# Optimization experiments

Measured on AMD Instinct MI355X. Metric: run time of the kernel, lower is better.

Reference implementation:

```python
import jax, jax.numpy as jnp
import numpy as np
from jax import lax

B, T, N, H = 2048, 128, 128, 256  # batch, timesteps, input_size (drivers), hidden_size


def setup_inputs() -> dict:
    key = jax.random.key(0)
    k = jax.random.split(key, 7)
    s = 0.05
    return {
        "input_data": jax.random.normal(k[0], (B, T, N), jnp.float32),
        "w_ih": jax.random.normal(k[1], (4 * H, N), jnp.float32) * s,   # PyTorch weight_ih_l0
        "w_hh": jax.random.normal(k[2], (4 * H, H), jnp.float32) * s,   # PyTorch weight_hh_l0
        "b_ih": jax.random.normal(k[3], (4 * H,), jnp.float32) * s,
        "b_hh": jax.random.normal(k[4], (4 * H,), jnp.float32) * s,
        "w_attn": jax.random.normal(k[5], (2 * H + T,), jnp.float32) * s,  # attn_linear weight (out=1)
        "b_attn": jax.random.normal(k[6], (1,), jnp.float32) * s,
    }


def reference(input_data, w_ih, w_hh, b_ih, b_hh, w_attn, b_attn):
    b, t_steps, n = input_data.shape
    h_dim = w_hh.shape[1]
    # Split attention weight: [h | c | driver-series] parts of the concat feature.
    w_h = w_attn[:h_dim]
    w_c = w_attn[h_dim:2 * h_dim]
    w_x = w_attn[2 * h_dim:]
    # Driver-series contribution to attn logits is time-invariant: [B, N]
    precomp = jnp.einsum("btn,t->bn", input_data, w_x)
    bias = b_attn[0]
    gate_bias = b_ih + b_hh

    xs = jnp.transpose(input_data, (1, 0, 2))  # [T, B, N]

    def step(carry, x_t):
        h, c = carry  # [B, H] each
        # hidden/cell are broadcast identically across the N drivers -> scalar per batch
        s = h @ w_h + c @ w_c                       # [B]
        logits = s[:, None] + precomp + bias        # [B, N]
        attn = jax.nn.softmax(logits, axis=1)       # [B, N]
        wx = attn * x_t                             # weighted input, [B, N]
        # PyTorch LSTM cell: gates ordered i, f, g, o
        gates = wx @ w_ih.T + h @ w_hh.T + gate_bias  # [B, 4H]
        i, f, g, o = jnp.split(gates, 4, axis=1)
        c_new = jax.nn.sigmoid(f) * c + jax.nn.sigmoid(i) * jnp.tanh(g)
        h_new = jax.nn.sigmoid(o) * jnp.tanh(c_new)
        return (h_new, c_new), (wx, h_new)

    h0 = jnp.zeros((b, h_dim), input_data.dtype)
    c0 = jnp.zeros((b, h_dim), input_data.dtype)
    _, (ws, hs) = lax.scan(step, (h0, c0), xs)
    input_weighted = jnp.transpose(ws, (1, 0, 2))  # [B, T, N]
    input_encoded = jnp.transpose(hs, (1, 0, 2))   # [B, T, H]
    return input_weighted, input_encoded
```

## Files before the change

### kernel.cpp

```cpp
#include <hip/hip_runtime.h>
#include <hip/hip_bf16.h>


#define B_ 2048
#define T_ 128
#define N_ 128
#define H_ 256
#define RG_ 64

typedef float f32x4 __attribute__((ext_vector_type(4)));
typedef short bf16x8 __attribute__((ext_vector_type(8)));
typedef unsigned short u16;
typedef unsigned int u32;
typedef u32 u32x4 __attribute__((ext_vector_type(4)));

__device__ __forceinline__ u16 f2bf(float f) {
  unsigned int u = __float_as_uint(f);
  u += 0x7fffu + ((u >> 16) & 1u);
  return (u16)(u >> 16);
}
__device__ __forceinline__ float sigm(float x) { return 1.f / (1.f + __expf(-x)); }
__device__ __forceinline__ float tanh_(float x) {
  float e = __expf(2.f * x);
  return 1.f - 2.f / (e + 1.f);
}

__device__ __forceinline__ bf16x8 ld16_dev(const u16* p) {
  bf16x8 v;
  asm volatile("global_load_dwordx4 %0, %1, off sc0 sc1" : "=v"(v) : "v"(p));
  return v;
}
__device__ __forceinline__ void st16_dev(u16* p, bf16x8 v) {
  asm volatile("global_store_dwordx4 %0, %1, off sc0 sc1" :: "v"(p), "v"(v) : "memory");
}
__device__ __forceinline__ void st1_dev(unsigned char* p, u32 v) {
  asm volatile("global_store_byte %0, %1, off sc0 sc1" :: "v"(p), "v"(v) : "memory");
}
__device__ __forceinline__ u32x4 ld_flags(const unsigned char* p) {
  u32x4 f;
  asm volatile("global_load_dwordx4 %0, %1, off sc0 sc1\n\ts_waitcnt vmcnt(0)"
               : "=v"(f) : "v"(p) : "memory");
  return f;
}

__global__ __launch_bounds__(128) void attn_wx_kernel(
    const float* __restrict__ x, const float* __restrict__ w_attn,
    float* __restrict__ out0) {
  const int b = blockIdx.x;
  const int n = threadIdx.x;
  const float* xb = x + (size_t)b * (T_ * N_);
  __shared__ float red[N_];
  float xv[T_];
  float p = 0.f;
#pragma unroll
  for (int t = 0; t < T_; ++t) {
    xv[t] = xb[t * N_ + n];
    p += xv[t] * w_attn[2 * H_ + t];
  }
  red[n] = p;
  __syncthreads();
  float m = red[0];
  for (int i = 1; i < N_; ++i) m = fmaxf(m, red[i]);
  float e = __expf(p - m);
  __syncthreads();
  red[n] = e;
  __syncthreads();
  float s = 0.f;
  for (int i = 0; i < N_; ++i) s += red[i];
  const float a = e / s;
  float* ob = out0 + (size_t)b * (T_ * N_);
#pragma unroll
  for (int t = 0; t < T_; ++t) ob[t * N_ + n] = a * xv[t];
}

__global__ __launch_bounds__(256) void prepack_kernel(
    const float* __restrict__ w_ih, const float* __restrict__ w_hh,
    u16* __restrict__ wpk) {
  const int idx = blockIdx.x * 256 + threadIdx.x;
  const int j = idx & 7;
  const int l = (idx >> 3) & 63;
  const int rest = idx >> 9;
  const int kc = rest % 12;
  const int wq = rest / 12;
  const int q = wq & 3;
  const int g16 = wq >> 2;
  const int grow = q * H_ + g16 * 16 + (l & 15);
  const int k = kc * 32 + ((l >> 4) << 3) + j;
  const float v = (k < N_) ? w_ih[(size_t)grow * N_ + k]
                           : w_hh[(size_t)grow * H_ + (k - N_)];
  wpk[idx] = f2bf(v);
}

__global__ __launch_bounds__(256, 1) void lstm_kernel(
    const float* __restrict__ wx,
    const u16* __restrict__ wpk,
    const float* __restrict__ b_ih, const float* __restrict__ b_hh,
    float* __restrict__ out1,
    u16* __restrict__ hx,
    unsigned char* __restrict__ flags) {
  __shared__ u16 hsh[2][32][72];
  const int bid = blockIdx.x;
  const int rg = bid >> 2, cg = bid & 3;
  const int rb = rg * 32;
  const int tid  = threadIdx.x;
  const int w    = tid >> 6;
  const int lane = tid & 63;
  const int l15  = lane & 15;
  const int koff = (lane >> 4) << 3;
  const int g16  = cg * 4 + w;
  const int hcol = cg * 64 + w * 16 + l15;

  bf16x8 wfrag[4][12];
  {
    const u16* wp = wpk + (size_t)(g16 * 48) * 512 + (size_t)lane * 8;
#pragma unroll
    for (int q = 0; q < 4; ++q)
#pragma unroll
      for (int kc = 0; kc < 12; ++kc)
        wfrag[q][kc] = *(const bf16x8*)(wp + (size_t)(q * 12 + kc) * 512);
  }
  float bias[4];
#pragma unroll
  for (int q = 0; q < 4; ++q)
    bias[q] = b_ih[q * H_ + hcol] + b_hh[q * H_ + hcol];
  float creg[2][4] = {};

  unsigned char* flrow  = flags + rg * 16;
  unsigned char* myflag = flrow + cg * 4 + w;
  const int mtf = w >> 1, kclf = w & 1;

  f32x4 pf[2][4][2];
#pragma unroll
  for (int mt = 0; mt < 2; ++mt)
#pragma unroll
    for (int kc = 0; kc < 4; ++kc) {
      const float* p = wx + (size_t)(rb + mt * 16 + l15) * (T_ * N_)
                          + kc * 32 + koff;
      pf[mt][kc][0] = *(const f32x4*)p;
      pf[mt][kc][1] = *(const f32x4*)(p + 4);
    }

  for (int t = 0; t < T_; ++t) {
    f32x4 acc[2][4];
#pragma unroll
    for (int mt = 0; mt < 2; ++mt)
#pragma unroll
      for (int q = 0; q < 4; ++q)
        acc[mt][q] = (f32x4){bias[q], bias[q], bias[q], bias[q]};

#pragma unroll
    for (int kc = 0; kc < 4; ++kc)
#pragma unroll
      for (int mt = 0; mt < 2; ++mt) {
        f32x4 x0 = pf[mt][kc][0], x1 = pf[mt][kc][1];
        bf16x8 a;
        a[0] = (short)f2bf(x0[0]); a[1] = (short)f2bf(x0[1]);
        a[2] = (short)f2bf(x0[2]); a[3] = (short)f2bf(x0[3]);
        a[4] = (short)f2bf(x1[0]); a[5] = (short)f2bf(x1[1]);
        a[6] = (short)f2bf(x1[2]); a[7] = (short)f2bf(x1[3]);
#pragma unroll
        for (int q = 0; q < 4; ++q)
          acc[mt][q] = __builtin_amdgcn_mfma_f32_16x16x32_bf16(a, wfrag[q][kc], acc[mt][q], 0, 0, 0);
      }
    if (t + 1 < T_) {
#pragma unroll
      for (int mt = 0; mt < 2; ++mt)
#pragma unroll
        for (int kc = 0; kc < 4; ++kc) {
          const float* p = wx + (size_t)(rb + mt * 16 + l15) * (T_ * N_)
                              + (size_t)(t + 1) * N_ + kc * 32 + koff;
          pf[mt][kc][0] = *(const f32x4*)p;
          pf[mt][kc][1] = *(const f32x4*)(p + 4);
        }
    }

    if (t > 0) {
      while (true) {
        u32x4 f = ld_flags(flrow);
        int ok = 1;
#pragma unroll
        for (int i = 0; i < 4; ++i) {
          u32 v = f[i];
          ok &= ((v & 255u) >= (u32)t) & (((v >> 8) & 255u) >= (u32)t) &
                (((v >> 16) & 255u) >= (u32)t) & (((v >> 24) & 255u) >= (u32)t);
        }
        if (ok) break;
      }
      __builtin_amdgcn_sched_barrier(0);

      const u16* hxr = hx + ((size_t)(t & 1) * RG_ + rg) * (4 * 4 * 512);
      bf16x8 ah[2][8];
#pragma unroll
      for (int mt = 0; mt < 2; ++mt)
#pragma unroll
        for (int kc2 = 0; kc2 < 8; ++kc2) {
          const int pc = kc2 >> 1, kcl = kc2 & 1;
          if (pc == cg)
            ah[mt][kc2] = *(const bf16x8*)&hsh[t & 1][mt * 16 + l15][kcl * 32 + koff];
          else
            ah[mt][kc2] = ld16_dev(hxr + ((size_t)pc * 4 + (mt * 2 + kcl)) * 512
                                       + (size_t)lane * 8);
        }
      asm volatile("s_waitcnt vmcnt(0)" ::: "memory");
      __builtin_amdgcn_sched_barrier(0);
#pragma unroll
      for (int kc2 = 0; kc2 < 8; ++kc2)
#pragma unroll
        for (int q = 0; q < 4; ++q)
#pragma unroll
          for (int mt = 0; mt < 2; ++mt)
            acc[mt][q] = __builtin_amdgcn_mfma_f32_16x16x32_bf16(ah[mt][kc2], wfrag[q][4 + kc2], acc[mt][q], 0, 0, 0);
    }

    const int nxt = (t + 1) & 1;
#pragma unroll
    for (int mt = 0; mt < 2; ++mt)
#pragma unroll
      for (int rr = 0; rr < 4; ++rr) {
        const float gi = acc[mt][0][rr];
        const float gf = acc[mt][1][rr];
        const float gg = acc[mt][2][rr];
        const float go = acc[mt][3][rr];
        const float c = sigm(gf) * creg[mt][rr] + sigm(gi) * tanh_(gg);
        creg[mt][rr] = c;
        const float h = sigm(go) * tanh_(c);
        const int row = mt * 16 + ((lane >> 4) << 2) + rr;
        out1[(size_t)(rb + row) * (T_ * H_) + (size_t)t * H_ + hcol] = h;
        hsh[nxt][row][w * 16 + l15] = f2bf(h);
      }
    __syncthreads();

    {
      bf16x8 fv = *(const bf16x8*)&hsh[nxt][mtf * 16 + l15][kclf * 32 + koff];
      u16* dst = hx + (((size_t)nxt * RG_ + rg) * 4 + cg) * (4 * 512)
                    + (size_t)w * 512 + (size_t)lane * 8;
      st16_dev(dst, fv);
      asm volatile("s_waitcnt vmcnt(0)" ::: "memory");
      if (lane == 0) st1_dev(myflag, (u32)(t + 1));
    }
  }
}

extern "C" void kernel_launch(void* const* d_in, const int* in_sizes, int n_in,
                              void* d_out, int out_size, void* d_ws, size_t ws_size,
                              hipStream_t stream) {
  const float* x      = (const float*)d_in[0];
  const float* w_ih   = (const float*)d_in[1];
  const float* w_hh   = (const float*)d_in[2];
  const float* b_ih   = (const float*)d_in[3];
  const float* b_hh   = (const float*)d_in[4];
  const float* w_attn = (const float*)d_in[5];

  float* out0 = (float*)d_out;
  float* out1 = out0 + (size_t)B_ * T_ * N_;

  unsigned char* flags = (unsigned char*)d_ws;
  u16* wpk = (u16*)((char*)d_ws + 16384);
  u16* hx  = (u16*)((char*)d_ws + 16384 + 786432);

  hipMemsetAsync(d_ws, 0, RG_ * 16, stream);
  prepack_kernel<<<dim3(1536), dim3(256), 0, stream>>>(w_ih, w_hh, wpk);
  attn_wx_kernel<<<dim3(B_), dim3(N_), 0, stream>>>(x, w_attn, out0);
  lstm_kernel<<<dim3(256), dim3(256), 0, stream>>>(out0, wpk, b_ih, b_hh,
                                                   out1, hx, flags);
}
```

Measured before the change: 961.2 us.

## Halve rows per LSTM block, double grid, stage inputs and peer h via LDS

Each LSTM block now handles 16 batch rows instead of 32, so the grid grows from 256 to 512 blocks at two blocks per CU. The next step's wx input is staged through a swizzled double-buffered LDS tile. Peer h fragments are loaded once per block by three waves into shared memory, not by every wave. The aim is to shorten the per-step serial critical path and cut redundant global loads. The cost is more flag-synchronising blocks, higher register pressure under launch_bounds(256,2), and an extra barrier per step.

```diff
diff --git a/kernel.cpp b/kernel.cpp
--- a/kernel.cpp
+++ b/kernel.cpp
@@ -6,13 +6,15 @@
 #define T_ 128
 #define N_ 128
 #define H_ 256
-#define RG_ 64
+#define MR_ 16
+#define RGN_ 128
 
 typedef float f32x4 __attribute__((ext_vector_type(4)));
 typedef short bf16x8 __attribute__((ext_vector_type(8)));
 typedef unsigned short u16;
 typedef unsigned int u32;
 typedef u32 u32x4 __attribute__((ext_vector_type(4)));
+typedef u16 u16x4 __attribute__((ext_vector_type(4)));
 
 __device__ __forceinline__ u16 f2bf(float f) {
   unsigned int u = __float_as_uint(f);
@@ -30,8 +32,8 @@
   asm volatile("global_load_dwordx4 %0, %1, off sc0 sc1" : "=v"(v) : "v"(p));
   return v;
 }
-__device__ __forceinline__ void st16_dev(u16* p, bf16x8 v) {
-  asm volatile("global_store_dwordx4 %0, %1, off sc0 sc1" :: "v"(p), "v"(v) : "memory");
+__device__ __forceinline__ void st8_dev(u16* p, u16x4 v) {
+  asm volatile("global_store_dwordx2 %0, %1, off sc0 sc1" :: "v"(p), "v"(v) : "memory");
 }
 __device__ __forceinline__ void st1_dev(unsigned char* p, u32 v) {
   asm volatile("global_store_byte %0, %1, off sc0 sc1" :: "v"(p), "v"(v) : "memory");
@@ -91,17 +93,20 @@
   wpk[idx] = f2bf(v);
 }
 
-__global__ __launch_bounds__(256, 1) void lstm_kernel(
+__global__ __launch_bounds__(256, 2) void lstm_kernel(
     const float* __restrict__ wx,
     const u16* __restrict__ wpk,
     const float* __restrict__ b_ih, const float* __restrict__ b_hh,
     float* __restrict__ out1,
     u16* __restrict__ hx,
     unsigned char* __restrict__ flags) {
-  __shared__ u16 hsh[2][32][72];
+  __shared__ float xstage[2][2048];
+  __shared__ u16 hsh[2][MR_][72];
+  __shared__ u16 fstage[8][512];
+
   const int bid = blockIdx.x;
   const int rg = bid >> 2, cg = bid & 3;
-  const int rb = rg * 32;
+  const int rb = rg * MR_;
   const int tid  = threadIdx.x;
   const int w    = tid >> 6;
   const int lane = tid & 63;
@@ -123,55 +128,64 @@
 #pragma unroll
   for (int q = 0; q < 4; ++q)
     bias[q] = b_ih[q * H_ + hcol] + b_hh[q * H_ + hcol];
-  float creg[2][4] = {};
+  float creg[4] = {};
 
   unsigned char* flrow  = flags + rg * 16;
   unsigned char* myflag = flrow + cg * 4 + w;
-  const int mtf = w >> 1, kclf = w & 1;
-
-  f32x4 pf[2][4][2];
-#pragma unroll
-  for (int mt = 0; mt < 2; ++mt)
+
+  int srow[2], scol[2];
+#pragma unroll
+  for (int i = 0; i < 2; ++i) {
+    const int d = w * 2048 + i * 1024 + lane * 16;
+    srow[i] = d >> 9;
+    scol[i] = ((((d >> 4) & 31) ^ (srow[i] & 7)) << 2);
+  }
+  const int e0 = w * 256 + lane * 4;
+  const int ef = e0 >> 9, er = e0 & 511;
+  const int erow = (er >> 3) & 15;
+  const int ecol = ((er >> 7) << 3) + (er & 7);
+
+  {
+    f32x4 v0 = *(const f32x4*)(wx + (size_t)(rb + srow[0]) * (T_ * N_) + scol[0]);
+    f32x4 v1 = *(const f32x4*)(wx + (size_t)(rb + srow[1]) * (T_ * N_) + scol[1]);
+    *(f32x4*)((char*)&xstage[0][0] + w * 2048 + lane * 16) = v0;
+    *(f32x4*)((char*)&xstage[0][0] + w * 2048 + 1024 + lane * 16) = v1;
+  }
+  __syncthreads();
+
+  const int rmask = l15 & 7;
+
+  for (int t = 0; t < T_; ++t) {
+    const int par = t & 1, np = par ^ 1;
+
+    f32x4 acc[4];
+#pragma unroll
+    for (int q = 0; q < 4; ++q)
+      acc[q] = (f32x4){bias[q], bias[q], bias[q], bias[q]};
+
 #pragma unroll
     for (int kc = 0; kc < 4; ++kc) {
-      const float* p = wx + (size_t)(rb + mt * 16 + l15) * (T_ * N_)
-                          + kc * 32 + koff;
-      pf[mt][kc][0] = *(const f32x4*)p;
-      pf[mt][kc][1] = *(const f32x4*)(p + 4);
-    }
-
-  for (int t = 0; t < T_; ++t) {
-    f32x4 acc[2][4];
-#pragma unroll
-    for (int mt = 0; mt < 2; ++mt)
+      const int g = kc * 8 + (koff >> 2);
+      const char* bp = (const char*)&xstage[par][0] + l15 * 512;
+      f32x4 x0 = *(const f32x4*)(bp + ((g ^ rmask) << 4));
+      f32x4 x1 = *(const f32x4*)(bp + (((g + 1) ^ rmask) << 4));
+      bf16x8 a;
+      a[0] = (short)f2bf(x0[0]); a[1] = (short)f2bf(x0[1]);
+      a[2] = (short)f2bf(x0[2]); a[3] = (short)f2bf(x0[3]);
+      a[4] = (short)f2bf(x1[0]); a[5] = (short)f2bf(x1[1]);
+      a[6] = (short)f2bf(x1[2]); a[7] = (short)f2bf(x1[3]);
 #pragma unroll
       for (int q = 0; q < 4; ++q)
-        acc[mt][q] = (f32x4){bias[q], bias[q], bias[q], bias[q]};
-
-#pragma unroll
-    for (int kc = 0; kc < 4; ++kc)
-#pragma unroll
-      for (int mt = 0; mt < 2; ++mt) {
-        f32x4 x0 = pf[mt][kc][0], x1 = pf[mt][kc][1];
-        bf16x8 a;
-        a[0] = (short)f2bf(x0[0]); a[1] = (short)f2bf(x0[1]);
-        a[2] = (short)f2bf(x0[2]); a[3] = (short)f2bf(x0[3]);
-        a[4] = (short)f2bf(x1[0]); a[5] = (short)f2bf(x1[1]);
-        a[6] = (short)f2bf(x1[2]); a[7] = (short)f2bf(x1[3]);
-#pragma unroll
-        for (int q = 0; q < 4; ++q)
-          acc[mt][q] = __builtin_amdgcn_mfma_f32_16x16x32_bf16(a, wfrag[q][kc], acc[mt][q], 0, 0, 0);
-      }
-    if (t + 1 < T_) {
-#pragma unroll
-      for (int mt = 0; mt < 2; ++mt)
-#pragma unroll
-        for (int kc = 0; kc < 4; ++kc) {
-          const float* p = wx + (size_t)(rb + mt * 16 + l15) * (T_ * N_)
-                              + (size_t)(t + 1) * N_ + kc * 32 + koff;
-          pf[mt][kc][0] = *(const f32x4*)p;
-          pf[mt][kc][1] = *(const f32x4*)(p + 4);
-        }
+        acc[q] = __builtin_amdgcn_mfma_f32_16x16x32_bf16(a, wfrag[q][kc], acc[q], 0, 0, 0);
+    }
+
+    f32x4 wv0, wv1;
+    const bool dowx = (t + 1 < T_);
+    if (dowx) {
+      const float* p0 = wx + (size_t)(rb + srow[0]) * (T_ * N_) + (size_t)(t + 1) * N_ + scol[0];
+      const float* p1 = wx + (size_t)(rb + srow[1]) * (T_ * N_) + (size_t)(t + 1) * N_ + scol[1];
+      wv0 = *(const f32x4*)p0;
+      wv1 = *(const f32x4*)p1;
     }
 
     if (t > 0) {
@@ -188,53 +202,61 @@
       }
       __builtin_amdgcn_sched_barrier(0);
 
-      const u16* hxr = hx + ((size_t)(t & 1) * RG_ + rg) * (4 * 4 * 512);
-      bf16x8 ah[2][8];
-#pragma unroll
-      for (int mt = 0; mt < 2; ++mt)
-#pragma unroll
-        for (int kc2 = 0; kc2 < 8; ++kc2) {
-          const int pc = kc2 >> 1, kcl = kc2 & 1;
-          if (pc == cg)
-            ah[mt][kc2] = *(const bf16x8*)&hsh[t & 1][mt * 16 + l15][kcl * 32 + koff];
-          else
-            ah[mt][kc2] = ld16_dev(hxr + ((size_t)pc * 4 + (mt * 2 + kcl)) * 512
-                                       + (size_t)lane * 8);
-        }
+      const u16* hxr = hx + ((size_t)par * RGN_ + rg) * 4096;
+      bf16x8 fv0, fv1;
+      int k0 = 0, k1 = 0;
+      if (w < 3) {
+        const int r0 = w * 2, r1 = w * 2 + 1;
+        k0 = (r0 < 2 * cg) ? r0 : r0 + 2;
+        k1 = (r1 < 2 * cg) ? r1 : r1 + 2;
+        fv0 = ld16_dev(hxr + k0 * 512 + lane * 8);
+        fv1 = ld16_dev(hxr + k1 * 512 + lane * 8);
+      }
       asm volatile("s_waitcnt vmcnt(0)" ::: "memory");
-      __builtin_amdgcn_sched_barrier(0);
-#pragma unroll
-      for (int kc2 = 0; kc2 < 8; ++kc2)
+      if (w < 3) {
+        *(bf16x8*)&fstage[k0][lane * 8] = fv0;
+        *(bf16x8*)&fstage[k1][lane * 8] = fv1;
+      }
+    }
+    if (dowx) {
+      *(f32x4*)((char*)&xstage[np][0] + w * 2048 + lane * 16) = wv0;
+      *(f32x4*)((char*)&xstage[np][0] + w * 2048 + 1024 + lane * 16) = wv1;
+    }
+
+    if (t > 0) {
+      __syncthreads();
+#pragma unroll
+      for (int kc2 = 0; kc2 < 8; ++kc2) {
+        bf16x8 a;
+        if ((kc2 >> 1) == cg)
+          a = *(const bf16x8*)&hsh[par][l15][(kc2 & 1) * 32 + koff];
+        else
+          a = *(const bf16x8*)&fstage[kc2][lane * 8];
 #pragma unroll
         for (int q = 0; q < 4; ++q)
-#pragma unroll
-          for (int mt = 0; mt < 2; ++mt)
-            acc[mt][q] = __builtin_amdgcn_mfma_f32_16x16x32_bf16(ah[mt][kc2], wfrag[q][4 + kc2], acc[mt][q], 0, 0, 0);
-    }
-
-    const int nxt = (t + 1) & 1;
-#pragma unroll
-    for (int mt = 0; mt < 2; ++mt)
-#pragma unroll
-      for (int rr = 0; rr < 4; ++rr) {
-        const float gi = acc[mt][0][rr];
-        const float gf = acc[mt][1][rr];
-        const float gg = acc[mt][2][rr];
-        const float go = acc[mt][3][rr];
-        const float c = sigm(gf) * creg[mt][rr] + sigm(gi) * tanh_(gg);
-        creg[mt][rr] = c;
-        const float h = sigm(go) * tanh_(c);
-        const int row = mt * 16 + ((lane >> 4) << 2) + rr;
-        out1[(size_t)(rb + row) * (T_ * H_) + (size_t)t * H_ + hcol] = h;
-        hsh[nxt][row][w * 16 + l15] = f2bf(h);
-      }
+          acc[q] = __builtin_amdgcn_mfma_f32_16x16x32_bf16(a, wfrag[q][4 + kc2], acc[q], 0, 0, 0);
+      }
+    }
+
+#pragma unroll
+    for (int rr = 0; rr < 4; ++rr) {
+      const float gi = acc[0][rr];
+      const float gf = acc[1][rr];
+      const float gg = acc[2][rr];
+      const float go = acc[3][rr];
+      const float c = sigm(gf) * creg[rr] + sigm(gi) * tanh_(gg);
+      creg[rr] = c;
+      const float h = sigm(go) * tanh_(c);
+      const int row = ((lane >> 4) << 2) + rr;
+      out1[(size_t)(rb + row) * (T_ * H_) + (size_t)t * H_ + hcol] = h;
+      hsh[np][row][w * 16 + l15] = f2bf(h);
+    }
     __syncthreads();
 
     {
-      bf16x8 fv = *(const bf16x8*)&hsh[nxt][mtf * 16 + l15][kclf * 32 + koff];
-      u16* dst = hx + (((size_t)nxt * RG_ + rg) * 4 + cg) * (4 * 512)
-                    + (size_t)w * 512 + (size_t)lane * 8;
-      st16_dev(dst, fv);
+      u16x4 v = *(const u16x4*)&hsh[np][erow][ef * 32 + ecol];
+      u16* dst = hx + ((size_t)np * RGN_ + rg) * 4096 + cg * 1024 + e0;
+      st8_dev(dst, v);
       asm volatile("s_waitcnt vmcnt(0)" ::: "memory");
       if (lane == 0) st1_dev(myflag, (u32)(t + 1));
     }
@@ -258,9 +280,9 @@
   u16* wpk = (u16*)((char*)d_ws + 16384);
   u16* hx  = (u16*)((char*)d_ws + 16384 + 786432);
 
-  hipMemsetAsync(d_ws, 0, RG_ * 16, stream);
+  hipMemsetAsync(d_ws, 0, RGN_ * 16, stream);
   prepack_kernel<<<dim3(1536), dim3(256), 0, stream>>>(w_ih, w_hh, wpk);
   attn_wx_kernel<<<dim3(B_), dim3(N_), 0, stream>>>(x, w_attn, out0);
-  lstm_kernel<<<dim3(256), dim3(256), 0, stream>>>(out0, wpk, b_ih, b_hh,
-                                                   out1, hx, flags);
-}
+  lstm_kernel<<<dim3(RGN_ * 4), dim3(256), 0, stream>>>(out0, wpk, b_ih, b_hh,
+                                                        out1, hx, flags);
+}
```

Measured after the change: 1.369 ms. 1.42x slower.

## Move input-projection MFMAs off the recurrence critical path and coalesce h stores

Applied to the files above, without the earlier changes.

Computes the next step's input-to-gate MFMAs (wx·W_ih) after publishing the current step's flag, so this work overlaps the wait for peer blocks instead of sitting before the spin. Hidden outputs are staged in shared memory and written to out1 as coalesced 16-byte stores rather than scattered scalar stores. The flag write now waits only on the hx store (vmcnt(2)) instead of draining all outstanding stores. Flag rows are padded to 128 bytes per row group so pollers of different groups do not share cache lines. The cost is extra LDS for staging and a more delicate ordering of memory operations across blocks.

```diff
diff --git a/kernel.cpp b/kernel.cpp
--- a/kernel.cpp
+++ b/kernel.cpp
@@ -99,6 +99,7 @@
     u16* __restrict__ hx,
     unsigned char* __restrict__ flags) {
   __shared__ u16 hsh[2][32][72];
+  __shared__ float osh[2][32][68];
   const int bid = blockIdx.x;
   const int rg = bid >> 2, cg = bid & 3;
   const int rb = rg * 32;
@@ -125,44 +126,60 @@
     bias[q] = b_ih[q * H_ + hcol] + b_hh[q * H_ + hcol];
   float creg[2][4] = {};
 
-  unsigned char* flrow  = flags + rg * 16;
+  unsigned char* flrow  = flags + (size_t)rg * 128;
   unsigned char* myflag = flrow + cg * 4 + w;
   const int mtf = w >> 1, kclf = w & 1;
 
   f32x4 pf[2][4][2];
+  f32x4 acc[2][4];
 #pragma unroll
   for (int mt = 0; mt < 2; ++mt)
 #pragma unroll
     for (int kc = 0; kc < 4; ++kc) {
-      const float* p = wx + (size_t)(rb + mt * 16 + l15) * (T_ * N_)
-                          + kc * 32 + koff;
+      const float* p = wx + (size_t)(rb + mt * 16 + l15) * (T_ * N_) + kc * 32 + koff;
       pf[mt][kc][0] = *(const f32x4*)p;
       pf[mt][kc][1] = *(const f32x4*)(p + 4);
     }
+#pragma unroll
+  for (int mt = 0; mt < 2; ++mt)
+#pragma unroll
+    for (int q = 0; q < 4; ++q)
+      acc[mt][q] = (f32x4){bias[q], bias[q], bias[q], bias[q]};
+#pragma unroll
+  for (int kc = 0; kc < 4; ++kc)
+#pragma unroll
+    for (int mt = 0; mt < 2; ++mt) {
+      f32x4 x0 = pf[mt][kc][0], x1 = pf[mt][kc][1];
+      bf16x8 a;
+      a[0] = (short)f2bf(x0[0]); a[1] = (short)f2bf(x0[1]);
+      a[2] = (short)f2bf(x0[2]); a[3] = (short)f2bf(x0[3]);
+      a[4] = (short)f2bf(x1[0]); a[5] = (short)f2bf(x1[1]);
+      a[6] = (short)f2bf(x1[2]); a[7] = (short)f2bf(x1[3]);
+#pragma unroll
+      for (int q = 0; q < 4; ++q)
+        acc[mt][q] = __builtin_amdgcn_mfma_f32_16x16x32_bf16(a, wfrag[q][kc], acc[mt][q], 0, 0, 0);
+    }
 
   for (int t = 0; t < T_; ++t) {
-    f32x4 acc[2][4];
-#pragma unroll
-    for (int mt = 0; mt < 2; ++mt)
-#pragma unroll
-      for (int q = 0; q < 4; ++q)
-        acc[mt][q] = (f32x4){bias[q], bias[q], bias[q], bias[q]};
-
-#pragma unroll
-    for (int kc = 0; kc < 4; ++kc)
-#pragma unroll
-      for (int mt = 0; mt < 2; ++mt) {
-        f32x4 x0 = pf[mt][kc][0], x1 = pf[mt][kc][1];
-        bf16x8 a;
-        a[0] = (short)f2bf(x0[0]); a[1] = (short)f2bf(x0[1]);
-        a[2] = (short)f2bf(x0[2]); a[3] = (short)f2bf(x0[3]);
-        a[4] = (short)f2bf(x1[0]); a[5] = (short)f2bf(x1[1]);
-        a[6] = (short)f2bf(x1[2]); a[7] = (short)f2bf(x1[3]);
-#pragma unroll
-        for (int q = 0; q < 4; ++q)
-          acc[mt][q] = __builtin_amdgcn_mfma_f32_16x16x32_bf16(a, wfrag[q][kc], acc[mt][q], 0, 0, 0);
+    const int par = t & 1, np = par ^ 1;
+
+    if (t > 0) {
+      while (true) {
+        u32x4 f = ld_flags(flrow);
+        int ok = 1;
+#pragma unroll
+        for (int i = 0; i < 4; ++i) {
+          u32 v = f[i];
+          ok &= ((v & 255u) >= (u32)t) & (((v >> 8) & 255u) >= (u32)t) &
+                (((v >> 16) & 255u) >= (u32)t) & (((v >> 24) & 255u) >= (u32)t);
+        }
+        if (ok) break;
       }
-    if (t + 1 < T_) {
+      __builtin_amdgcn_sched_barrier(0);
+    }
+
+    const bool dowx = (t + 1 < T_);
+    if (dowx) {
 #pragma unroll
       for (int mt = 0; mt < 2; ++mt)
 #pragma unroll
@@ -173,22 +190,8 @@
           pf[mt][kc][1] = *(const f32x4*)(p + 4);
         }
     }
-
     if (t > 0) {
-      while (true) {
-        u32x4 f = ld_flags(flrow);
-        int ok = 1;
-#pragma unroll
-        for (int i = 0; i < 4; ++i) {
-          u32 v = f[i];
-          ok &= ((v & 255u) >= (u32)t) & (((v >> 8) & 255u) >= (u32)t) &
-                (((v >> 16) & 255u) >= (u32)t) & (((v >> 24) & 255u) >= (u32)t);
-        }
-        if (ok) break;
-      }
-      __builtin_amdgcn_sched_barrier(0);
-
-      const u16* hxr = hx + ((size_t)(t & 1) * RG_ + rg) * (4 * 4 * 512);
+      const u16* hxr = hx + ((size_t)par * RG_ + rg) * 8192;
       bf16x8 ah[2][8];
 #pragma unroll
       for (int mt = 0; mt < 2; ++mt)
@@ -196,7 +199,7 @@
         for (int kc2 = 0; kc2 < 8; ++kc2) {
           const int pc = kc2 >> 1, kcl = kc2 & 1;
           if (pc == cg)
-            ah[mt][kc2] = *(const bf16x8*)&hsh[t & 1][mt * 16 + l15][kcl * 32 + koff];
+            ah[mt][kc2] = *(const bf16x8*)&hsh[par][mt * 16 + l15][kcl * 32 + koff];
           else
             ah[mt][kc2] = ld16_dev(hxr + ((size_t)pc * 4 + (mt * 2 + kcl)) * 512
                                        + (size_t)lane * 8);
@@ -210,9 +213,10 @@
 #pragma unroll
           for (int mt = 0; mt < 2; ++mt)
             acc[mt][q] = __builtin_amdgcn_mfma_f32_16x16x32_bf16(ah[mt][kc2], wfrag[q][4 + kc2], acc[mt][q], 0, 0, 0);
-    }
-
-    const int nxt = (t + 1) & 1;
+    } else {
+      asm volatile("s_waitcnt vmcnt(0)" ::: "memory");
+    }
+
 #pragma unroll
     for (int mt = 0; mt < 2; ++mt)
 #pragma unroll
@@ -225,18 +229,47 @@
         creg[mt][rr] = c;
         const float h = sigm(go) * tanh_(c);
         const int row = mt * 16 + ((lane >> 4) << 2) + rr;
-        out1[(size_t)(rb + row) * (T_ * H_) + (size_t)t * H_ + hcol] = h;
-        hsh[nxt][row][w * 16 + l15] = f2bf(h);
+        osh[par][row][w * 16 + l15] = h;
+        hsh[np][row][w * 16 + l15] = f2bf(h);
       }
     __syncthreads();
 
     {
-      bf16x8 fv = *(const bf16x8*)&hsh[nxt][mtf * 16 + l15][kclf * 32 + koff];
-      u16* dst = hx + (((size_t)nxt * RG_ + rg) * 4 + cg) * (4 * 512)
-                    + (size_t)w * 512 + (size_t)lane * 8;
+      bf16x8 fv = *(const bf16x8*)&hsh[np][mtf * 16 + l15][kclf * 32 + koff];
+      u16* dst = hx + ((size_t)np * RG_ + rg) * 8192 + (size_t)(cg * 4 + w) * 512
+                    + (size_t)lane * 8;
       st16_dev(dst, fv);
-      asm volatile("s_waitcnt vmcnt(0)" ::: "memory");
-      if (lane == 0) st1_dev(myflag, (u32)(t + 1));
+    }
+#pragma unroll
+    for (int i = 0; i < 2; ++i) {
+      const int row = w * 8 + (lane >> 4) + i * 4;
+      float* op = out1 + (size_t)(rb + row) * (T_ * H_) + (size_t)t * H_
+                       + cg * 64 + l15 * 4;
+      *(f32x4*)op = *(const f32x4*)&osh[par][row][l15 * 4];
+    }
+    asm volatile("s_waitcnt vmcnt(2)" ::: "memory");
+    if (lane == 0) st1_dev(myflag, (u32)(t + 1));
+
+    if (dowx) {
+#pragma unroll
+      for (int mt = 0; mt < 2; ++mt)
+#pragma unroll
+        for (int q = 0; q < 4; ++q)
+          acc[mt][q] = (f32x4){bias[q], bias[q], bias[q], bias[q]};
+#pragma unroll
+      for (int kc = 0; kc < 4; ++kc)
+#pragma unroll
+        for (int mt = 0; mt < 2; ++mt) {
+          f32x4 x0 = pf[mt][kc][0], x1 = pf[mt][kc][1];
+          bf16x8 a;
+          a[0] = (short)f2bf(x0[0]); a[1] = (short)f2bf(x0[1]);
+          a[2] = (short)f2bf(x0[2]); a[3] = (short)f2bf(x0[3]);
+          a[4] = (short)f2bf(x1[0]); a[5] = (short)f2bf(x1[1]);
+          a[6] = (short)f2bf(x1[2]); a[7] = (short)f2bf(x1[3]);
+#pragma unroll
+          for (int q = 0; q < 4; ++q)
+            acc[mt][q] = __builtin_amdgcn_mfma_f32_16x16x32_bf16(a, wfrag[q][kc], acc[mt][q], 0, 0, 0);
+        }
     }
   }
 }
@@ -255,10 +288,10 @@
   float* out1 = out0 + (size_t)B_ * T_ * N_;
 
   unsigned char* flags = (unsigned char*)d_ws;
-  u16* wpk = (u16*)((char*)d_ws + 16384);
-  u16* hx  = (u16*)((char*)d_ws + 16384 + 786432);
-
-  hipMemsetAsync(d_ws, 0, RG_ * 16, stream);
+  u16* wpk  = (u16*)((char*)d_ws + 16384);
+  u16* hx   = (u16*)((char*)d_ws + 16384 + 786432);
+
+  hipMemsetAsync(flags, 0, 8192, stream);
   prepack_kernel<<<dim3(1536), dim3(256), 0, stream>>>(w_ih, w_hh, wpk);
   attn_wx_kernel<<<dim3(B_), dim3(N_), 0, stream>>>(x, w_attn, out0);
   lstm_kernel<<<dim3(256), dim3(256), 0, stream>>>(out0, wpk, b_ih, b_hh,
```

Result: faster. 829.4 us (-13.7%).
